# Optimization experiments

Measured on AMD Instinct MI355X. Metric: run time of the kernel, lower is better.

## Reference

```python
import jax, jax.numpy as jnp
import numpy as np

B = 8192          # batch
CIN = 256         # in_channels
COUT = 64         # out_channels
K = 3             # kernel_size
NK = 4            # num_kernels
HIDDEN = int(CIN * 0.25)   # attention hidden = int(in_channels*ratio) = 64
TEMP = 34.0       # attention temperature
KAN_IN = 64 * 4   # base*4 = flattened conv output (COUT*2*2)
GRID_SIZE, SPLINE_ORDER = 5, 3
GMIN, GMAX = -1.0, 1.0
NUM_BASES = GRID_SIZE + SPLINE_ORDER  # 8


def setup_inputs() -> dict:
    key = jax.random.key(0)
    ks = jax.random.split(key, 8)
    s = 0.05
    return {
        "x": jax.random.normal(ks[0], (B, CIN, 4, 4), jnp.float32),
        # dynamic-conv kernel bank [num_kernels, out, in, k, k]
        "weight": jax.random.normal(ks[1], (NK, COUT, CIN, K, K), jnp.float32) * s,
        "bias": jnp.zeros((NK, COUT), jnp.float32),
        # Attention2D: GAP -> fc1 (1x1 conv == linear) -> ReLU -> fc2 -> softmax(/T)
        "fc1_w": jax.random.normal(ks[2], (HIDDEN, CIN), jnp.float32) * s,
        "fc1_b": jnp.zeros((HIDDEN,), jnp.float32),
        "fc2_w": jax.random.normal(ks[3], (NK, HIDDEN), jnp.float32) * s,
        "fc2_b": jnp.zeros((NK,), jnp.float32),
        # KANLinear params (efficient-KAN style)
        "kan_base_w": jax.random.normal(ks[4], (COUT, KAN_IN), jnp.float32) * s,
        "kan_spline_w": jax.random.normal(ks[5], (COUT, KAN_IN, NUM_BASES), jnp.float32) * s,
        "kan_spline_scaler": jnp.ones((COUT, KAN_IN), jnp.float32),
    }


def _bspline_bases(x):
    """Cox-de Boor B-spline bases; x [B, F] -> [B, F, GRID_SIZE+SPLINE_ORDER]."""
    h = (GMAX - GMIN) / GRID_SIZE
    # extended grid, shared across features: length grid_size + 2*order + 1 = 12
    grid = jnp.arange(-SPLINE_ORDER, GRID_SIZE + SPLINE_ORDER + 1, dtype=x.dtype) * h + GMIN
    xe = x[..., None]  # [B, F, 1]
    bases = ((xe >= grid[:-1]) & (xe < grid[1:])).astype(x.dtype)  # order 0
    for k in range(1, SPLINE_ORDER + 1):
        left = (xe - grid[: -(k + 1)]) / (grid[k:-1] - grid[: -(k + 1)]) * bases[..., :-1]
        right = (grid[k + 1:] - xe) / (grid[k + 1:] - grid[1:-k]) * bases[..., 1:]
        bases = left + right
    return bases  # [B, F, 8]


def reference(x, weight, bias, fc1_w, fc1_b, fc2_w, fc2_b,
              kan_base_w, kan_spline_w, kan_spline_scaler):
    b = x.shape[0]
    # --- Attention2D: softmax over kernel bank ---
    pooled = x.mean(axis=(2, 3))                                  # [B, CIN]
    hid = jax.nn.relu(pooled @ fc1_w.T + fc1_b)                   # [B, HIDDEN]
    attn = jax.nn.softmax((hid @ fc2_w.T + fc2_b) / TEMP, axis=-1)  # [B, NK]
    # --- per-sample dynamic conv, fused form ---
    # sum_k a[b,k] * conv(x, W_k) == conv with per-sample aggregated weight
    w_all = weight.reshape(NK * COUT, CIN, K, K)
    y = jax.lax.conv_general_dilated(
        x, w_all, window_strides=(1, 1), padding="VALID",
        dimension_numbers=("NCHW", "OIHW", "NCHW"))                # [B, NK*COUT, 2, 2]
    y = y.reshape(b, NK, COUT, y.shape[-2], y.shape[-1])
    conv_out = jnp.einsum("bk,bkohw->bohw", attn, y)
    conv_out = conv_out + (attn @ bias)[:, :, None, None]          # aggregated bias
    # --- KANLinear on flattened conv output ---
    feat = conv_out.reshape(b, -1)                                 # [B, 256]
    base_out = jax.nn.silu(feat) @ kan_base_w.T                    # [B, COUT]
    bases = _bspline_bases(feat)                                   # [B, 256, 8]
    spline_out = jnp.einsum("big,oig->bo", bases,
                            kan_spline_w * kan_spline_scaler[..., None])
    return base_out + spline_out                                   # [B, COUT]
```

## Files before the change

kernel.cpp:

```cpp
#include <hip/hip_runtime.h>

#define BT   8192
#define CINC 256
#define HID  64
#define NKC  4
#define MS   16

typedef _Float16 half8  __attribute__((ext_vector_type(8)));
typedef _Float16 half4v __attribute__((ext_vector_type(4)));
typedef _Float16 half2v __attribute__((ext_vector_type(2)));
typedef float    floatx4  __attribute__((ext_vector_type(4)));
typedef float    floatx16 __attribute__((ext_vector_type(16)));

__global__ __launch_bounds__(256) void w3_transform(
    const float* __restrict__ weight, _Float16* __restrict__ W3)
{
    const int n = blockIdx.x;
    const int c = threadIdx.x;
    const float* src = weight + ((size_t)n * 256 + c) * 9;
    const int cc = c >> 5, ci = c & 31;
    #pragma unroll
    for (int ij = 0; ij < 9; ++ij) {
        W3[((size_t)(cc * 9 + ij) * 256 + n) * 32 + ci] = (_Float16)src[ij];
    }
}

__global__ __launch_bounds__(256) void wk3_transform(
    const float* __restrict__ base_w, const float* __restrict__ spline_w,
    const float* __restrict__ scaler, _Float16* __restrict__ Wk3)
{
    const int st = blockIdx.x;
    const int tid = threadIdx.x;
    #pragma unroll
    for (int u = 0; u < 8; ++u) {
        const int idx = u * 256 + tid;
        const int n = idx >> 5, kk = idx & 31;
        const int k = st * 32 + kk;
        float v;
        if (k < 256) {
            v = base_w[n * 256 + k];
        } else {
            const int r = k - 256;
            const int i = r >> 3, g = r & 7;
            v = spline_w[((size_t)n * 256 + i) * 8 + g] * scaler[n * 256 + i];
        }
        Wk3[(size_t)st * 2048 + idx] = (_Float16)v;
    }
}

__device__ __forceinline__ void bases8(float xv, _Float16* dst) {
    float g[12];
    #pragma unroll
    for (int u = 0; u < 12; ++u) g[u] = (float)(u - 3) * 0.4f - 1.0f;
    float t0[11];
    #pragma unroll
    for (int t = 0; t < 11; ++t)
        t0[t] = (xv >= g[t] && xv < g[t + 1]) ? 1.f : 0.f;
    float t1[10];
    #pragma unroll
    for (int t = 0; t < 10; ++t)
        t1[t] = (xv - g[t]) / (g[t + 1] - g[t]) * t0[t]
              + (g[t + 2] - xv) / (g[t + 2] - g[t + 1]) * t0[t + 1];
    float t2[9];
    #pragma unroll
    for (int t = 0; t < 9; ++t)
        t2[t] = (xv - g[t]) / (g[t + 2] - g[t]) * t1[t]
              + (g[t + 3] - xv) / (g[t + 3] - g[t + 1]) * t1[t + 1];
    half8 hb;
    #pragma unroll
    for (int t = 0; t < 8; ++t) {
        float b = (xv - g[t]) / (g[t + 3] - g[t]) * t2[t]
                + (g[t + 4] - xv) / (g[t + 4] - g[t + 1]) * t2[t + 1];
        hb[t] = (_Float16)b;
    }
    *(half8*)dst = hb;
}

__global__ __launch_bounds__(256, 2) void fused_kernel(
    const float* __restrict__ x, const _Float16* __restrict__ W3,
    const _Float16* __restrict__ Wk3, const float* __restrict__ bias,
    const float* __restrict__ fc1_w, const float* __restrict__ fc1_b,
    const float* __restrict__ fc2_w, const float* __restrict__ fc2_b,
    float* __restrict__ out)
{
    __shared__ __align__(16) char smem[16 * 2312 * 2];
    __shared__ float hid_lds[16 * 68];
    __shared__ float attn_s[16][4];

    _Float16* Xs   = (_Float16*)smem;
    float*    pooled = (float*)(smem + 20992);
    _Float16* Act  = (_Float16*)smem;

    const int tid = threadIdx.x;
    const int wv = tid >> 6, lane = tid & 63;
    const int nl = lane & 15, q = lane >> 4;
    const int b0 = blockIdx.x * MS;

    const int posr = nl & 3;
    const int aLane = (nl >> 2) * 656 + ((posr >> 1) * 4 + (posr & 1)) * 40 + q * 8;
    int lbW[4];
    #pragma unroll
    for (int kb = 0; kb < 4; ++kb) lbW[kb] = ((wv + 4 * kb) * 16 + nl) * 32 + q * 8;

    const int xs_ = tid >> 4, xcp = tid & 15;
    const float* xg = x + ((size_t)(b0 + xs_) * 256 + xcp * 2) * 16;
    _Float16* xd = &Xs[xs_ * 656 + xcp * 2];
    float* pd = &pooled[xs_ * 260 + xcp * 2];

    floatx4 acc[4][4];
    #pragma unroll
    for (int rt = 0; rt < 4; ++rt)
        #pragma unroll
        for (int kb = 0; kb < 4; ++kb) acc[rt][kb] = floatx4{0.f, 0.f, 0.f, 0.f};

    floatx16 r0 = *(const floatx16*)(xg);
    floatx16 r1 = *(const floatx16*)(xg + 16);

    for (int cc = 0; cc < 8; ++cc) {
        __syncthreads();
        #pragma unroll
        for (int p = 0; p < 16; ++p) {
            half2v h;
            h[0] = (_Float16)r0[p];
            h[1] = (_Float16)r1[p];
            *(half2v*)&xd[p * 40] = h;
        }
        {
            float s0 = 0.f, s1 = 0.f;
            #pragma unroll
            for (int p = 0; p < 16; ++p) { s0 += r0[p]; s1 += r1[p]; }
            pd[cc * 32] = s0 * (1.0f / 16.0f);
            pd[cc * 32 + 1] = s1 * (1.0f / 16.0f);
        }
        if (cc < 7) {
            r0 = *(const floatx16*)(xg + (cc + 1) * 512);
            r1 = *(const floatx16*)(xg + (cc + 1) * 512 + 16);
        }
        __syncthreads();

        #pragma unroll 3
        for (int ij = 0; ij < 9; ++ij) {
            const int step = cc * 9 + ij;
            const int p0 = (ij / 3) * 4 + (ij % 3);
            const _Float16* wstep = W3 + (size_t)step * 8192;
            half8 bF[4];
            #pragma unroll
            for (int kb = 0; kb < 4; ++kb) bF[kb] = *(const half8*)(wstep + lbW[kb]);
            half8 aF[4];
            #pragma unroll
            for (int rt = 0; rt < 4; ++rt) aF[rt] = *(const half8*)&Xs[rt * 2624 + aLane + p0 * 40];
            #pragma unroll
            for (int rt = 0; rt < 4; ++rt)
                #pragma unroll
                for (int kb = 0; kb < 4; ++kb)
                    acc[rt][kb] = __builtin_amdgcn_mfma_f32_16x16x32_f16(aF[rt], bF[kb], acc[rt][kb], 0, 0, 0);
        }
    }

    {
        float facc[4];
        #pragma unroll
        for (int p = 0; p < 4; ++p) {
            const int h = wv * 16 + p * 4 + q;
            float a = fc1_b[h];
            const float4* wr = (const float4*)(fc1_w + h * 256);
            const float4* pr = (const float4*)(pooled + nl * 260);
            #pragma unroll 8
            for (int c4 = 0; c4 < 64; ++c4) {
                const float4 w = wr[c4], pv = pr[c4];
                a += w.x * pv.x + w.y * pv.y + w.z * pv.z + w.w * pv.w;
            }
            facc[p] = fmaxf(a, 0.f);
        }
        #pragma unroll
        for (int p = 0; p < 4; ++p) hid_lds[nl * 68 + wv * 16 + p * 4 + q] = facc[p];
    }
    __syncthreads();
    if (wv == 0) {
        const int s = lane >> 2, kb = lane & 3;
        float l = fc2_b[kb];
        #pragma unroll 8
        for (int h = 0; h < 64; ++h) l += hid_lds[s * 68 + h] * fc2_w[kb * 64 + h];
        float m = fmaxf(l, __shfl_xor(l, 1));
        m = fmaxf(m, __shfl_xor(m, 2));
        const float e = __expf((l - m) * (1.0f / 34.0f));
        float sm = e + __shfl_xor(e, 1);
        sm += __shfl_xor(sm, 2);
        attn_s[s][kb] = e / sm;
    }
    __syncthreads();

    {
        const int o = wv * 16 + nl;
        const float bb0 = bias[o], bb1 = bias[64 + o], bb2 = bias[128 + o], bb3 = bias[192 + o];
        #pragma unroll
        for (int rt = 0; rt < 4; ++rt) {
            const int s = rt * 4 + q;
            const float a0 = attn_s[s][0], a1 = attn_s[s][1], a2 = attn_s[s][2], a3 = attn_s[s][3];
            const float badd = a0 * bb0 + a1 * bb1 + a2 * bb2 + a3 * bb3;
            float f[4];
            #pragma unroll
            for (int e = 0; e < 4; ++e)
                f[e] = a0 * acc[rt][0][e] + a1 * acc[rt][1][e]
                     + a2 * acc[rt][2][e] + a3 * acc[rt][3][e] + badd;
            half4v sv;
            #pragma unroll
            for (int e = 0; e < 4; ++e) sv[e] = (_Float16)(f[e] / (1.f + __expf(-f[e])));
            *(half4v*)&Act[s * 2312 + o * 4] = sv;
            #pragma unroll
            for (int e = 0; e < 4; ++e)
                bases8(f[e], &Act[s * 2312 + 256 + (o * 4 + e) * 8]);
        }
    }
    __syncthreads();

    {
        floatx4 acc2 = floatx4{0.f, 0.f, 0.f, 0.f};
        const _Float16* wkb = Wk3 + ((size_t)(wv * 16 + nl) * 32 + q * 8);
        const _Float16* ab = &Act[nl * 2312 + q * 8];
        #pragma unroll 8
        for (int st = 0; st < 72; ++st) {
            const half8 aF = *(const half8*)(ab + st * 32);
            const half8 bF = *(const half8*)(wkb + (size_t)st * 2048);
            acc2 = __builtin_amdgcn_mfma_f32_16x16x32_f16(aF, bF, acc2, 0, 0, 0);
        }
        #pragma unroll
        for (int reg = 0; reg < 4; ++reg)
            out[(size_t)(b0 + q * 4 + reg) * 64 + wv * 16 + nl] = acc2[reg];
    }
}

extern "C" void kernel_launch(void* const* d_in, const int* in_sizes, int n_in,
                              void* d_out, int out_size, void* d_ws, size_t ws_size,
                              hipStream_t stream) {
    const float* x          = (const float*)d_in[0];
    const float* weight     = (const float*)d_in[1];
    const float* bias       = (const float*)d_in[2];
    const float* fc1_w      = (const float*)d_in[3];
    const float* fc1_b      = (const float*)d_in[4];
    const float* fc2_w      = (const float*)d_in[5];
    const float* fc2_b      = (const float*)d_in[6];
    const float* kan_base_w = (const float*)d_in[7];
    const float* kan_spline = (const float*)d_in[8];
    const float* kan_scaler = (const float*)d_in[9];
    float* out = (float*)d_out;

    _Float16* W3  = (_Float16*)d_ws;
    _Float16* Wk3 = W3 + (size_t)72 * 8192;

    w3_transform<<<256, 256, 0, stream>>>(weight, W3);
    wk3_transform<<<72, 256, 0, stream>>>(kan_base_w, kan_spline, kan_scaler, Wk3);
    fused_kernel<<<BT / MS, 256, 0, stream>>>(x, W3, Wk3, bias, fc1_w, fc1_b,
                                              fc2_w, fc2_b, out);
}
```

Measured before the change: 306.9 us.

## Use 512-thread blocks, split conv and KAN work across waves, MFMA attention fc1

Doubles the block to 8 waves. Each wave now covers half the sample rows in the conv MFMA loop and half the K range in the KAN GEMM, and the two halves are reduced through LDS. The fc1 attention layer is moved from scalar fp32 dot products to fp16 MFMA, using a pre-transformed fc1 weight, and the pooled input is stored as fp16. B-spline and SiLU math swap divisions for reciprocal multiplies. This aims at more parallelism and latency hiding per CU, at the cost of an extra sync and reduced precision in the attention path.

```diff
diff --git a/kernel.cpp b/kernel.cpp
--- a/kernel.cpp
+++ b/kernel.cpp
@@ -1,14 +1,10 @@
 #include <hip/hip_runtime.h>
 
 #define BT   8192
-#define CINC 256
-#define HID  64
-#define NKC  4
 #define MS   16
 
 typedef _Float16 half8  __attribute__((ext_vector_type(8)));
 typedef _Float16 half4v __attribute__((ext_vector_type(4)));
-typedef _Float16 half2v __attribute__((ext_vector_type(2)));
 typedef float    floatx4  __attribute__((ext_vector_type(4)));
 typedef float    floatx16 __attribute__((ext_vector_type(16)));
 
@@ -27,24 +23,35 @@
 
 __global__ __launch_bounds__(256) void wk3_transform(
     const float* __restrict__ base_w, const float* __restrict__ spline_w,
-    const float* __restrict__ scaler, _Float16* __restrict__ Wk3)
+    const float* __restrict__ scaler, const float* __restrict__ fc1_w,
+    _Float16* __restrict__ Wk3, _Float16* __restrict__ Wf3)
 {
     const int st = blockIdx.x;
     const int tid = threadIdx.x;
-    #pragma unroll
-    for (int u = 0; u < 8; ++u) {
-        const int idx = u * 256 + tid;
-        const int n = idx >> 5, kk = idx & 31;
-        const int k = st * 32 + kk;
-        float v;
-        if (k < 256) {
-            v = base_w[n * 256 + k];
-        } else {
-            const int r = k - 256;
-            const int i = r >> 3, g = r & 7;
-            v = spline_w[((size_t)n * 256 + i) * 8 + g] * scaler[n * 256 + i];
-        }
-        Wk3[(size_t)st * 2048 + idx] = (_Float16)v;
+    if (st < 72) {
+        #pragma unroll
+        for (int u = 0; u < 8; ++u) {
+            const int idx = u * 256 + tid;
+            const int n = idx >> 5, kk = idx & 31;
+            const int k = st * 32 + kk;
+            float v;
+            if (k < 256) {
+                v = base_w[n * 256 + k];
+            } else {
+                const int r = k - 256;
+                const int i = r >> 3, g = r & 7;
+                v = spline_w[((size_t)n * 256 + i) * 8 + g] * scaler[n * 256 + i];
+            }
+            Wk3[(size_t)st * 2048 + idx] = (_Float16)v;
+        }
+    } else {
+        const int st2 = st - 72;
+        #pragma unroll
+        for (int u = 0; u < 8; ++u) {
+            const int idx = u * 256 + tid;
+            const int n = idx >> 5, kk = idx & 31;
+            Wf3[(size_t)st2 * 2048 + idx] = (_Float16)fc1_w[n * 256 + st2 * 32 + kk];
+        }
     }
 }
 
@@ -52,6 +59,9 @@
     float g[12];
     #pragma unroll
     for (int u = 0; u < 12; ++u) g[u] = (float)(u - 3) * 0.4f - 1.0f;
+    float dt[12];
+    #pragma unroll
+    for (int u = 0; u < 12; ++u) dt[u] = xv - g[u];
     float t0[11];
     #pragma unroll
     for (int t = 0; t < 11; ++t)
@@ -59,27 +69,27 @@
     float t1[10];
     #pragma unroll
     for (int t = 0; t < 10; ++t)
-        t1[t] = (xv - g[t]) / (g[t + 1] - g[t]) * t0[t]
-              + (g[t + 2] - xv) / (g[t + 2] - g[t + 1]) * t0[t + 1];
+        t1[t] = dt[t] * (1.0f / (g[t + 1] - g[t])) * t0[t]
+              - dt[t + 2] * (1.0f / (g[t + 2] - g[t + 1])) * t0[t + 1];
     float t2[9];
     #pragma unroll
     for (int t = 0; t < 9; ++t)
-        t2[t] = (xv - g[t]) / (g[t + 2] - g[t]) * t1[t]
-              + (g[t + 3] - xv) / (g[t + 3] - g[t + 1]) * t1[t + 1];
+        t2[t] = dt[t] * (1.0f / (g[t + 2] - g[t])) * t1[t]
+              - dt[t + 3] * (1.0f / (g[t + 3] - g[t + 1])) * t1[t + 1];
     half8 hb;
     #pragma unroll
     for (int t = 0; t < 8; ++t) {
-        float b = (xv - g[t]) / (g[t + 3] - g[t]) * t2[t]
-                + (g[t + 4] - xv) / (g[t + 4] - g[t + 1]) * t2[t + 1];
+        float b = dt[t] * (1.0f / (g[t + 3] - g[t])) * t2[t]
+                - dt[t + 4] * (1.0f / (g[t + 4] - g[t + 1])) * t2[t + 1];
         hb[t] = (_Float16)b;
     }
     *(half8*)dst = hb;
 }
 
-__global__ __launch_bounds__(256, 2) void fused_kernel(
+__global__ __launch_bounds__(512, 4) void fused_kernel(
     const float* __restrict__ x, const _Float16* __restrict__ W3,
-    const _Float16* __restrict__ Wk3, const float* __restrict__ bias,
-    const float* __restrict__ fc1_w, const float* __restrict__ fc1_b,
+    const _Float16* __restrict__ Wk3, const _Float16* __restrict__ Wf3,
+    const float* __restrict__ bias, const float* __restrict__ fc1_b,
     const float* __restrict__ fc2_w, const float* __restrict__ fc2_b,
     float* __restrict__ out)
 {
@@ -87,55 +97,45 @@
     __shared__ float hid_lds[16 * 68];
     __shared__ float attn_s[16][4];
 
-    _Float16* Xs   = (_Float16*)smem;
-    float*    pooled = (float*)(smem + 20992);
-    _Float16* Act  = (_Float16*)smem;
+    _Float16* Xs  = (_Float16*)smem;
+    _Float16* Pl  = (_Float16*)(smem + 20992);
+    _Float16* Act = (_Float16*)smem;
 
     const int tid = threadIdx.x;
     const int wv = tid >> 6, lane = tid & 63;
     const int nl = lane & 15, q = lane >> 4;
+    const int cg = wv & 3, rh = wv >> 2;
     const int b0 = blockIdx.x * MS;
 
     const int posr = nl & 3;
     const int aLane = (nl >> 2) * 656 + ((posr >> 1) * 4 + (posr & 1)) * 40 + q * 8;
     int lbW[4];
     #pragma unroll
-    for (int kb = 0; kb < 4; ++kb) lbW[kb] = ((wv + 4 * kb) * 16 + nl) * 32 + q * 8;
-
-    const int xs_ = tid >> 4, xcp = tid & 15;
-    const float* xg = x + ((size_t)(b0 + xs_) * 256 + xcp * 2) * 16;
-    _Float16* xd = &Xs[xs_ * 656 + xcp * 2];
-    float* pd = &pooled[xs_ * 260 + xcp * 2];
-
-    floatx4 acc[4][4];
-    #pragma unroll
-    for (int rt = 0; rt < 4; ++rt)
-        #pragma unroll
-        for (int kb = 0; kb < 4; ++kb) acc[rt][kb] = floatx4{0.f, 0.f, 0.f, 0.f};
-
-    floatx16 r0 = *(const floatx16*)(xg);
-    floatx16 r1 = *(const floatx16*)(xg + 16);
+    for (int kb = 0; kb < 4; ++kb) lbW[kb] = ((cg + 4 * kb) * 16 + nl) * 32 + q * 8;
+
+    const int s_ = tid >> 5, cch = tid & 31;
+    const float* xg = x + ((size_t)(b0 + s_) * 256 + cch) * 16;
+    _Float16* xd = &Xs[s_ * 656 + cch];
+
+    floatx4 acc[2][4];
+    #pragma unroll
+    for (int rr = 0; rr < 2; ++rr)
+        #pragma unroll
+        for (int kb = 0; kb < 4; ++kb) acc[rr][kb] = floatx4{0.f, 0.f, 0.f, 0.f};
+
+    floatx16 r = *(const floatx16*)xg;
 
     for (int cc = 0; cc < 8; ++cc) {
         __syncthreads();
         #pragma unroll
-        for (int p = 0; p < 16; ++p) {
-            half2v h;
-            h[0] = (_Float16)r0[p];
-            h[1] = (_Float16)r1[p];
-            *(half2v*)&xd[p * 40] = h;
-        }
+        for (int p = 0; p < 16; ++p) xd[p * 40] = (_Float16)r[p];
         {
-            float s0 = 0.f, s1 = 0.f;
-            #pragma unroll
-            for (int p = 0; p < 16; ++p) { s0 += r0[p]; s1 += r1[p]; }
-            pd[cc * 32] = s0 * (1.0f / 16.0f);
-            pd[cc * 32 + 1] = s1 * (1.0f / 16.0f);
-        }
-        if (cc < 7) {
-            r0 = *(const floatx16*)(xg + (cc + 1) * 512);
-            r1 = *(const floatx16*)(xg + (cc + 1) * 512 + 16);
-        }
+            float sm = 0.f;
+            #pragma unroll
+            for (int p = 0; p < 16; ++p) sm += r[p];
+            Pl[s_ * 264 + cc * 32 + cch] = (_Float16)(sm * (1.0f / 16.0f));
+        }
+        if (cc < 7) r = *(const floatx16*)(xg + (cc + 1) * 512);
         __syncthreads();
 
         #pragma unroll 3
@@ -146,36 +146,36 @@
             half8 bF[4];
             #pragma unroll
             for (int kb = 0; kb < 4; ++kb) bF[kb] = *(const half8*)(wstep + lbW[kb]);
-            half8 aF[4];
-            #pragma unroll
-            for (int rt = 0; rt < 4; ++rt) aF[rt] = *(const half8*)&Xs[rt * 2624 + aLane + p0 * 40];
-            #pragma unroll
-            for (int rt = 0; rt < 4; ++rt)
+            half8 aF[2];
+            #pragma unroll
+            for (int rr = 0; rr < 2; ++rr)
+                aF[rr] = *(const half8*)&Xs[(rh * 2 + rr) * 2624 + aLane + p0 * 40];
+            #pragma unroll
+            for (int rr = 0; rr < 2; ++rr)
                 #pragma unroll
                 for (int kb = 0; kb < 4; ++kb)
-                    acc[rt][kb] = __builtin_amdgcn_mfma_f32_16x16x32_f16(aF[rt], bF[kb], acc[rt][kb], 0, 0, 0);
-        }
-    }
-
-    {
-        float facc[4];
-        #pragma unroll
-        for (int p = 0; p < 4; ++p) {
-            const int h = wv * 16 + p * 4 + q;
-            float a = fc1_b[h];
-            const float4* wr = (const float4*)(fc1_w + h * 256);
-            const float4* pr = (const float4*)(pooled + nl * 260);
-            #pragma unroll 8
-            for (int c4 = 0; c4 < 64; ++c4) {
-                const float4 w = wr[c4], pv = pr[c4];
-                a += w.x * pv.x + w.y * pv.y + w.z * pv.z + w.w * pv.w;
-            }
-            facc[p] = fmaxf(a, 0.f);
-        }
-        #pragma unroll
-        for (int p = 0; p < 4; ++p) hid_lds[nl * 68 + wv * 16 + p * 4 + q] = facc[p];
+                    acc[rr][kb] = __builtin_amdgcn_mfma_f32_16x16x32_f16(aF[rr], bF[kb], acc[rr][kb], 0, 0, 0);
+        }
+    }
+
+    if (rh == 0) {
+        floatx4 a1 = floatx4{0.f, 0.f, 0.f, 0.f};
+        const _Float16* wfb = Wf3 + ((cg * 16 + nl) * 32 + q * 8);
+        const _Float16* pb = &Pl[nl * 264 + q * 8];
+        #pragma unroll
+        for (int st = 0; st < 8; ++st) {
+            const half8 aF = *(const half8*)(pb + st * 32);
+            const half8 bF = *(const half8*)(wfb + st * 2048);
+            a1 = __builtin_amdgcn_mfma_f32_16x16x32_f16(aF, bF, a1, 0, 0, 0);
+        }
+        const int h = cg * 16 + nl;
+        const float fb = fc1_b[h];
+        #pragma unroll
+        for (int reg = 0; reg < 4; ++reg)
+            hid_lds[(q * 4 + reg) * 68 + h] = fmaxf(a1[reg] + fb, 0.f);
     }
     __syncthreads();
+
     if (wv == 0) {
         const int s = lane >> 2, kb = lane & 3;
         float l = fc2_b[kb];
@@ -191,21 +191,24 @@
     __syncthreads();
 
     {
-        const int o = wv * 16 + nl;
+        const int o = cg * 16 + nl;
         const float bb0 = bias[o], bb1 = bias[64 + o], bb2 = bias[128 + o], bb3 = bias[192 + o];
         #pragma unroll
-        for (int rt = 0; rt < 4; ++rt) {
-            const int s = rt * 4 + q;
+        for (int rr = 0; rr < 2; ++rr) {
+            const int s = (rh * 2 + rr) * 4 + q;
             const float a0 = attn_s[s][0], a1 = attn_s[s][1], a2 = attn_s[s][2], a3 = attn_s[s][3];
             const float badd = a0 * bb0 + a1 * bb1 + a2 * bb2 + a3 * bb3;
             float f[4];
             #pragma unroll
             for (int e = 0; e < 4; ++e)
-                f[e] = a0 * acc[rt][0][e] + a1 * acc[rt][1][e]
-                     + a2 * acc[rt][2][e] + a3 * acc[rt][3][e] + badd;
+                f[e] = a0 * acc[rr][0][e] + a1 * acc[rr][1][e]
+                     + a2 * acc[rr][2][e] + a3 * acc[rr][3][e] + badd;
             half4v sv;
             #pragma unroll
-            for (int e = 0; e < 4; ++e) sv[e] = (_Float16)(f[e] / (1.f + __expf(-f[e])));
+            for (int e = 0; e < 4; ++e) {
+                const float ex = __expf(-f[e]);
+                sv[e] = (_Float16)(f[e] * __builtin_amdgcn_rcpf(1.f + ex));
+            }
             *(half4v*)&Act[s * 2312 + o * 4] = sv;
             #pragma unroll
             for (int e = 0; e < 4; ++e)
@@ -215,18 +218,25 @@
     __syncthreads();
 
     {
-        floatx4 acc2 = floatx4{0.f, 0.f, 0.f, 0.f};
-        const _Float16* wkb = Wk3 + ((size_t)(wv * 16 + nl) * 32 + q * 8);
+        floatx4 a2 = floatx4{0.f, 0.f, 0.f, 0.f};
+        const _Float16* wkb = Wk3 + ((size_t)(cg * 16 + nl) * 32 + q * 8);
         const _Float16* ab = &Act[nl * 2312 + q * 8];
-        #pragma unroll 8
-        for (int st = 0; st < 72; ++st) {
+        #pragma unroll 6
+        for (int i = 0; i < 36; ++i) {
+            const int st = rh * 36 + i;
             const half8 aF = *(const half8*)(ab + st * 32);
             const half8 bF = *(const half8*)(wkb + (size_t)st * 2048);
-            acc2 = __builtin_amdgcn_mfma_f32_16x16x32_f16(aF, bF, acc2, 0, 0, 0);
-        }
-        #pragma unroll
-        for (int reg = 0; reg < 4; ++reg)
-            out[(size_t)(b0 + q * 4 + reg) * 64 + wv * 16 + nl] = acc2[reg];
+            a2 = __builtin_amdgcn_mfma_f32_16x16x32_f16(aF, bF, a2, 0, 0, 0);
+        }
+        if (rh == 1) *(floatx4*)&hid_lds[cg * 256 + lane * 4] = a2;
+        __syncthreads();
+        if (rh == 0) {
+            const floatx4 p = *(const floatx4*)&hid_lds[cg * 256 + lane * 4];
+            a2 = a2 + p;
+            #pragma unroll
+            for (int reg = 0; reg < 4; ++reg)
+                out[(size_t)(b0 + q * 4 + reg) * 64 + cg * 16 + nl] = a2[reg];
+        }
     }
 }
 
@@ -247,9 +257,11 @@
 
     _Float16* W3  = (_Float16*)d_ws;
     _Float16* Wk3 = W3 + (size_t)72 * 8192;
+    _Float16* Wf3 = Wk3 + (size_t)72 * 2048;
 
     w3_transform<<<256, 256, 0, stream>>>(weight, W3);
-    wk3_transform<<<72, 256, 0, stream>>>(kan_base_w, kan_spline, kan_scaler, Wk3);
-    fused_kernel<<<BT / MS, 256, 0, stream>>>(x, W3, Wk3, bias, fc1_w, fc1_b,
+    wk3_transform<<<80, 256, 0, stream>>>(kan_base_w, kan_spline, kan_scaler,
+                                          fc1_w, Wk3, Wf3);
+    fused_kernel<<<BT / MS, 512, 0, stream>>>(x, W3, Wk3, Wf3, bias, fc1_b,
                                               fc2_w, fc2_b, out);
 }
```

Measured after the change: 276.6 us. 9.9% less time.
